# Kernel tuning notes

Measured on AMD Instinct MI355X. Metric: run time of the kernel, lower is better.

## Reference

```python
import jax, jax.numpy as jnp
import numpy as np

EPS = 1e-6
SCAL = 5.0
PARTS = 16
NFEAT = 32
RES = 64


def conv(x, w, b, stride=1):
    y = jax.lax.conv_general_dilated(x, w, (stride, stride), 'SAME',
                                     dimension_numbers=('NCHW', 'OIHW', 'NCHW'))
    return y + b[None, :, None, None]


def spatial_softmax(x):
    b, k, h, w = x.shape
    return jax.nn.softmax(x.reshape(b, k, h * w), axis=-1).reshape(b, k, h, w)


def make_grid(h, w):
    ys = jnp.linspace(-1.0, 1.0, h)
    xs = jnp.linspace(-1.0, 1.0, w)
    gy, gx = jnp.meshgrid(ys, xs, indexing='ij')
    return jnp.stack([gy, gx], axis=-1)  # [h, w, 2]


def e_sigma(x, w1, b1, w2, b2, wp, bp):
    # shared shape/appearance encoder: parts via spatial softmax + residual sum map
    h1 = jax.nn.relu(conv(x, w1, b1, stride=2))   # [B,64,64,64]
    h2 = jax.nn.relu(conv(h1, w2, b2))            # [B,64,64,64]
    parts = spatial_softmax(conv(h2, wp, bp))     # [B,16,64,64]
    return parts, h2


def e_alpha(x, w1, b1, w2, b2):
    h1 = jax.nn.relu(conv(x, w1, b1))
    return conv(h1, w2, b2)                       # [B,32,64,64]


def get_mu_and_prec(parts):
    # soft-argmax mean + 2x2 covariance -> inverse Cholesky factor L_inv
    b, k, h, w = parts.shape
    grid = make_grid(h, w)
    mu = jnp.einsum('bkhw,hwc->bkc', parts, grid)                       # [b,k,2]
    outer = jnp.einsum('hwm,hwn->hwmn', grid, grid)
    cov = jnp.einsum('bkhw,hwmn->bkmn', parts, outer) - jnp.einsum('bkm,bkn->bkmn', mu, mu)
    a = jnp.sqrt(cov[..., 0, 0] + EPS)
    bb = cov[..., 0, 1] / (a + EPS)
    c = jnp.sqrt(jnp.maximum(cov[..., 1, 1] - bb * bb, 0.0) + EPS)
    det = a * c
    z = jnp.zeros_like(a)
    L_inv = SCAL / (det[..., None, None] + EPS) * jnp.stack(
        [jnp.stack([c, z], axis=-1), jnp.stack([-bb, a], axis=-1)], axis=-2)  # [b,k,2,2]
    return mu, L_inv


def feat_mu_to_enc(alpha, mu, L_inv, h, w):
    # render Cauchy-shaped part heatmaps from (mu, L_inv) and paint part features
    grid = make_grid(h, w)
    dist = grid[None, None] - mu[:, :, None, None, :]        # [b,k,h,w,2]
    proj = jnp.einsum('bkhwi,bkij->bkhwj', dist, L_inv)
    heat = 1.0 / (1.0 + jnp.sum(proj * proj, axis=-1))       # [b,k,h,w]
    norm = heat / (jnp.sum(heat, axis=(2, 3), keepdims=True) + EPS)
    fmap = jnp.einsum('bkf,bkhw->bfhw', alpha, norm)         # [b,nf,h,w]
    return jnp.concatenate([heat, fmap], axis=1)             # [b,nk+nf,h,w]


def decoder(enc, w1, b1, w2, b2, w3, b3):
    h1 = jax.nn.relu(conv(enc, w1, b1))                      # [B,64,64,64]
    up = jnp.repeat(jnp.repeat(h1, 2, axis=2), 2, axis=3)    # nearest upsample -> 128
    h2 = jax.nn.relu(conv(up, w2, b2))
    return jax.nn.sigmoid(conv(h2, w3, b3))                  # [B,3,128,128]


def setup_inputs():
    key = jax.random.key(0)
    ks = jax.random.split(key, 16)
    def w(k, shape):
        fan_in = shape[1] * shape[2] * shape[3]
        return (jax.random.normal(k, shape, jnp.float32) / np.sqrt(fan_in)).astype(jnp.float32)
    B = 32
    return {
        'x': jax.random.uniform(ks[0], (B, 3, 128, 128), jnp.float32),
        'x_spatial_transform': jax.random.uniform(ks[1], (B, 3, 128, 128), jnp.float32),
        'x_appearance_transform': jax.random.uniform(ks[2], (B, 3, 128, 128), jnp.float32),
        'coord': jax.random.normal(ks[3], (B, PARTS, 2), jnp.float32) * 0.5,
        'vector': jax.random.normal(ks[4], (B, PARTS, 2), jnp.float32) * 0.1,
        'es_w1': w(ks[5], (RES, 3, 3, 3)), 'es_b1': jnp.zeros((RES,), jnp.float32),
        'es_w2': w(ks[6], (RES, RES, 3, 3)), 'es_b2': jnp.zeros((RES,), jnp.float32),
        'es_wp': w(ks[7], (PARTS, RES, 3, 3)), 'es_bp': jnp.zeros((PARTS,), jnp.float32),
        'ea_w1': w(ks[8], (RES, RES, 3, 3)), 'ea_b1': jnp.zeros((RES,), jnp.float32),
        'ea_w2': w(ks[9], (NFEAT, RES, 3, 3)), 'ea_b2': jnp.zeros((NFEAT,), jnp.float32),
        'd_w1': w(ks[10], (RES, PARTS + NFEAT, 3, 3)), 'd_b1': jnp.zeros((RES,), jnp.float32),
        'd_w2': w(ks[11], (32, RES, 3, 3)), 'd_b2': jnp.zeros((32,), jnp.float32),
        'd_w3': w(ks[12], (3, 32, 3, 3)), 'd_b3': jnp.zeros((3,), jnp.float32),
    }


def reference(x, x_spatial_transform, x_appearance_transform, coord, vector,
              es_w1, es_b1, es_w2, es_b2, es_wp, es_bp,
              ea_w1, ea_b1, ea_w2, ea_b2,
              d_w1, d_b1, d_w2, d_b2, d_w3, d_b3):
    # shape stream (appearance-transformed image -> geometry)
    shape_parts, _ = e_sigma(x_appearance_transform, es_w1, es_b1, es_w2, es_b2, es_wp, es_bp)
    mu, L_inv = get_mu_and_prec(shape_parts)
    # appearance stream (spatially-transformed image -> appearance)
    app_parts, app_sum = e_sigma(x_spatial_transform, es_w1, es_b1, es_w2, es_b2, es_wp, es_bp)
    f_xs = e_alpha(app_sum, ea_w1, ea_b1, ea_w2, ea_b2)
    # local part appearances: gather features under each part map
    alpha = jnp.einsum('bfhw,bkhw->bkf', f_xs, app_parts)
    encoding = feat_mu_to_enc(alpha, mu, L_inv, 64, 64)
    reconstruction = decoder(encoding, d_w1, d_b1, d_w2, d_b2, d_w3, d_b3)
    # composite loss
    mu_a, L_inv_a = get_mu_and_prec(app_parts)
    rec_loss = jnp.mean((x - reconstruction) ** 2)
    equiv_loss = jnp.mean((mu - mu_a) ** 2) + 0.01 * jnp.mean((L_inv - L_inv_a) ** 2)
    transport_loss = jnp.mean((mu_a - (coord + vector)) ** 2)
    loss = rec_loss + equiv_loss + transport_loss
    return reconstruction, loss
```

## Files before the change

### kernel.cpp

```cpp
#include <hip/hip_runtime.h>
#include <hip/hip_bf16.h>

#define EPS 1e-6f
#define SCAL 5.0f

typedef __attribute__((ext_vector_type(8))) short bf8v;
typedef __attribute__((ext_vector_type(4))) float f32x4;

#define OFF_MU     0
#define OFF_LINV   1024
#define OFF_MUA    3072
#define OFF_LINVA  4096
#define OFF_HSUM   6144
#define OFF_ALPHA  6656
#define OFF_REC    23040
#define OFF_R1     32768
#define OFF_R2     (OFF_R1 + 8388608)
#define OFF_R3     (OFF_R2 + 8388608)
#define WS_TOTAL   (OFF_R3 + 16777216)

#define BA_XA   ((size_t)2 * OFF_R3)
#define BA_X2   ((size_t)2 * OFF_R1)
#define OFF_PARTSF OFF_R2
#define OFF_PROBS  (OFF_R2 + 4194304)
#define BA_EA1  ((size_t)2 * OFF_R3)
#define OFF_FXS (OFF_R3 + 4194304)
#define BA_E    ((size_t)2 * OFF_R2)
#define BA_D1   ((size_t)2 * OFF_R1)
#define BA_D2   ((size_t)2 * OFF_R3)

#define WT_ESW1 0
#define WT_ESB1 1728
#define WT_ESB2 1792
#define WT_ESBP 1856
#define WT_EAB1 1872
#define WT_EAB2 1936
#define WT_DB1  1968
#define WT_DB2  2032
#define WT_W3P  2064
#define WT_DB3  2928
#define P_WP2  0
#define P_WPP  36864
#define P_WPA1 46080
#define P_WPA2 82944
#define P_WPD1 101376
#define P_WPD2 138240

__device__ __attribute__((aligned(16))) float g_ws[WS_TOTAL];
__device__ __attribute__((aligned(16))) float g_wt[3072];
__device__ __attribute__((aligned(16))) __hip_bfloat16 g_wp[156672];
__device__ int g_isbf16;

__device__ __forceinline__ float selz(bool c, float v) { return c ? v : 0.f; }
__device__ __forceinline__ float cvtbf(short s) {
    return __uint_as_float(((unsigned int)(unsigned short)s) << 16);
}
__device__ __forceinline__ float ldin(const void* p, size_t i, int bf) {
    return bf ? __bfloat162float(((const __hip_bfloat16*)p)[i])
              : ((const float*)p)[i];
}

__device__ __forceinline__ float block_sum(float v) {
    __shared__ float sb[8];
    for (int off = 32; off; off >>= 1) v += __shfl_down(v, off, 64);
    int lane = threadIdx.x & 63, wid = threadIdx.x >> 6;
    __syncthreads();
    if (lane == 0) sb[wid] = v;
    __syncthreads();
    float r = 0.f;
    for (int i = 0; i < 4; ++i) r += sb[i];
    return r;
}
__device__ __forceinline__ float block_max(float v) {
    __shared__ float sb[8];
    for (int off = 32; off; off >>= 1) v = fmaxf(v, __shfl_down(v, off, 64));
    int lane = threadIdx.x & 63, wid = threadIdx.x >> 6;
    __syncthreads();
    if (lane == 0) sb[wid] = v;
    __syncthreads();
    float r = -1e30f;
    for (int i = 0; i < 4; ++i) r = fmaxf(r, sb[i]);
    return r;
}

__global__ void detect_k(const void* x) {
    const __hip_bfloat16* p = (const __hip_bfloat16*)x;
    int lane = threadIdx.x & 63;
    float v = 0.f;
    for (int i = lane; i < 256; i += 64) {
        float a = fabsf(__bfloat162float(p[i]));
        if (!(a <= 2.0f)) v = 1.f;
    }
    for (int off = 32; off; off >>= 1) v += __shfl_down(v, off, 64);
    if (lane == 0) {
        g_isbf16 = (v == 0.f) ? 1 : 0;
        g_ws[OFF_REC] = 0.f;
    }
}

__global__ void wpack_k(const void* esw1, const void* esb1, const void* esw2, const void* esb2,
                        const void* eswp, const void* esbp, const void* eaw1, const void* eab1,
                        const void* eaw2, const void* eab2, const void* dw1, const void* db1,
                        const void* dw2, const void* db2, const void* dw3, const void* db3) {
    int bf = g_isbf16;
    int gid0 = blockIdx.x * 256 + threadIdx.x, stride = gridDim.x * 256;
    for (int g = gid0; g < 1728; g += stride) g_wt[WT_ESW1 + g] = ldin(esw1, g, bf);
    for (int g = gid0; g < 64; g += stride) g_wt[WT_ESB1 + g] = ldin(esb1, g, bf);
    for (int g = gid0; g < 64; g += stride) g_wt[WT_ESB2 + g] = ldin(esb2, g, bf);
    for (int g = gid0; g < 16; g += stride) g_wt[WT_ESBP + g] = ldin(esbp, g, bf);
    for (int g = gid0; g < 64; g += stride) g_wt[WT_EAB1 + g] = ldin(eab1, g, bf);
    for (int g = gid0; g < 32; g += stride) g_wt[WT_EAB2 + g] = ldin(eab2, g, bf);
    for (int g = gid0; g < 64; g += stride) g_wt[WT_DB1 + g] = ldin(db1, g, bf);
    for (int g = gid0; g < 32; g += stride) g_wt[WT_DB2 + g] = ldin(db2, g, bf);
    for (int g = gid0; g < 3; g += stride) g_wt[WT_DB3 + g] = ldin(db3, g, bf);
    for (int g = gid0; g < 864; g += stride) {
        int t = g / 96, o = (g / 32) % 3, k = g & 31;
        g_wt[WT_W3P + g] = ldin(dw3, (size_t)(o * 32 + k) * 9 + t, bf);
    }
    for (int g = gid0; g < 36864; g += stride) {
        int t = g >> 12, n = (g >> 6) & 63, k = g & 63;
        g_wp[P_WP2 + g] = __float2bfloat16(ldin(esw2, (size_t)(n * 64 + k) * 9 + t, bf));
    }
    for (int g = gid0; g < 9216; g += stride) {
        int t = g >> 10, n = (g >> 6) & 15, k = g & 63;
        g_wp[P_WPP + g] = __float2bfloat16(ldin(eswp, (size_t)(n * 64 + k) * 9 + t, bf));
    }
    for (int g = gid0; g < 36864; g += stride) {
        int t = g >> 12, n = (g >> 6) & 63, k = g & 63;
        g_wp[P_WPA1 + g] = __float2bfloat16(ldin(eaw1, (size_t)(n * 64 + k) * 9 + t, bf));
    }
    for (int g = gid0; g < 18432; g += stride) {
        int t = g >> 11, n = (g >> 6) & 31, k = g & 63;
        g_wp[P_WPA2 + g] = __float2bfloat16(ldin(eaw2, (size_t)(n * 64 + k) * 9 + t, bf));
    }
    for (int g = gid0; g < 36864; g += stride) {
        int t = g >> 12, n = (g >> 6) & 63, k = g & 63;
        float v = (k < 48) ? ldin(dw1, (size_t)(n * 48 + k) * 9 + t, bf) : 0.f;
        g_wp[P_WPD1 + g] = __float2bfloat16(v);
    }
    for (int g = gid0; g < 18432; g += stride) {
        int t = g >> 11, n = (g >> 6) & 31, k = g & 63;
        g_wp[P_WPD2 + g] = __float2bfloat16(ldin(dw2, (size_t)(n * 64 + k) * 9 + t, bf));
    }
}

__global__ void __launch_bounds__(256)
conv_s2n_k(const void* __restrict__ inA, const void* __restrict__ inB) {
    int bf = g_isbf16;
    int tile = blockIdx.x & 15;
    int gb = blockIdx.x >> 4;
    int g = gb & 3, b = gb >> 2;
    const void* in = (b < 32) ? inA : inB;
    int bb = b & 31;
    int pix = tile * 256 + threadIdx.x;
    int y = pix >> 6, x = pix & 63;
    size_t inb = (size_t)bb * 3 * 16384;
    const float* W = g_wt + WT_ESW1 + (size_t)(g * 16) * 27;
    float acc[16];
    #pragma unroll
    for (int o = 0; o < 16; ++o) acc[o] = g_wt[WT_ESB1 + g * 16 + o];
    int iy0 = 2 * y, ix0 = 2 * x;
    bool my2 = (iy0 + 2 < 128), mx2 = (ix0 + 2 < 128);
    int iy2 = my2 ? iy0 + 2 : 127, ix2 = mx2 ? ix0 + 2 : 127;
    for (int ic = 0; ic < 3; ++ic) {
        size_t pb = inb + ic * 16384;
        float t[9];
        t[0] = ldin(in, pb + iy0 * 128 + ix0, bf);
        t[1] = ldin(in, pb + iy0 * 128 + ix0 + 1, bf);
        t[2] = selz(mx2, ldin(in, pb + iy0 * 128 + ix2, bf));
        t[3] = ldin(in, pb + (iy0 + 1) * 128 + ix0, bf);
        t[4] = ldin(in, pb + (iy0 + 1) * 128 + ix0 + 1, bf);
        t[5] = selz(mx2, ldin(in, pb + (iy0 + 1) * 128 + ix2, bf));
        t[6] = selz(my2, ldin(in, pb + iy2 * 128 + ix0, bf));
        t[7] = selz(my2, ldin(in, pb + iy2 * 128 + ix0 + 1, bf));
        t[8] = selz(my2 && mx2, ldin(in, pb + iy2 * 128 + ix2, bf));
        #pragma unroll
        for (int o = 0; o < 16; ++o) {
            const float* wr = W + (o * 3 + ic) * 9;
            float a = acc[o];
            #pragma unroll
            for (int j = 0; j < 9; ++j) a = fmaf(t[j], wr[j], a);
            acc[o] = a;
        }
    }
    __hip_bfloat16* out = (__hip_bfloat16*)g_ws + BA_XA + ((size_t)b * 4096 + pix) * 64 + g * 16;
    #pragma unroll
    for (int o = 0; o < 16; ++o) out[o] = __float2bfloat16(fmaxf(acc[o], 0.f));
}

__device__ __forceinline__ void stage_tile(__hip_bfloat16* sA,
                                           const __hip_bfloat16* __restrict__ inb, int y0) {
    for (int g = threadIdx.x; g < 3072; g += 256) {
        int r = g >> 9;
        int rem = g & 511;
        int px = rem >> 3, j = rem & 7;
        int yy = y0 - 1 + r;
        int P = px + 1;
        bf8v v = (bf8v){0, 0, 0, 0, 0, 0, 0, 0};
        if (yy >= 0 && yy <= 63)
            v = *(const bf8v*)(inb + ((size_t)(yy * 64 + px) * 64 + j * 8));
        *(bf8v*)(sA + ((r * 66 + P) * 64 + ((j ^ (P & 7)) * 8))) = v;
    }
    if (threadIdx.x < 96) {
        int g = threadIdx.x;
        int r = g / 16, rem = g % 16, side = rem >> 3, j = rem & 7;
        int P = side ? 65 : 0;
        *(bf8v*)(sA + ((r * 66 + P) * 64 + ((j ^ (P & 7)) * 8))) = (bf8v){0, 0, 0, 0, 0, 0, 0, 0};
    }
}

template<int TOTN, int NS, int OUTF32, int RELU>
__device__ __forceinline__ void conv_body(const __hip_bfloat16* sA, int bO, int y,
                                          int wid, int l15, int quad,
                                          int wp_off, int bias_off, size_t out_off) {
    f32x4 acc[4][NS];
    #pragma unroll
    for (int ms = 0; ms < 4; ++ms)
        #pragma unroll
        for (int ns = 0; ns < NS; ++ns) acc[ms][ns] = (f32x4){0.f, 0.f, 0.f, 0.f};

    if constexpr (NS == 1) {
        bf8v bw[18];
        #pragma unroll
        for (int it = 0; it < 18; ++it) {
            const int t = it >> 1, c = it & 1;
            bw[it] = *(const bf8v*)(g_wp + wp_off +
                     ((size_t)(t * TOTN + l15) * 64 + c * 32 + quad * 8));
        }
        #pragma unroll
        for (int it = 0; it < 18; ++it) {
            const int t = it >> 1, c = it & 1;
            const int dy = t / 3 - 1, dx = t % 3 - 1;
            const int r = wid + 1 + dy;
            const int j = c * 4 + quad;
            #pragma unroll
            for (int ms = 0; ms < 4; ++ms) {
                int P = ms * 16 + l15 + dx + 1;
                bf8v a = *(const bf8v*)(sA + ((r * 66 + P) * 64 + ((j ^ (P & 7)) * 8)));
                acc[ms][0] = __builtin_amdgcn_mfma_f32_16x16x32_bf16(a, bw[it], acc[ms][0], 0, 0, 0);
            }
        }
    } else {
        bf8v bq[2][NS];
        #pragma unroll
        for (int ns = 0; ns < NS; ++ns)
            bq[0][ns] = *(const bf8v*)(g_wp + wp_off +
                        ((size_t)(ns * 16 + l15) * 64 + quad * 8));
        #pragma unroll
        for (int it = 0; it < 18; ++it) {
            const int t = it >> 1, c = it & 1;
            if (it + 1 < 18) {
                const int t2 = (it + 1) >> 1, c2 = (it + 1) & 1;
                #pragma unroll
                for (int ns = 0; ns < NS; ++ns)
                    bq[(it + 1) & 1][ns] = *(const bf8v*)(g_wp + wp_off +
                        ((size_t)(t2 * TOTN + ns * 16 + l15) * 64 + c2 * 32 + quad * 8));
            }
            const int dy = t / 3 - 1, dx = t % 3 - 1;
            const int r = wid + 1 + dy;
            const int j = c * 4 + quad;
            bf8v a[4];
            #pragma unroll
            for (int ms = 0; ms < 4; ++ms) {
                int P = ms * 16 + l15 + dx + 1;
                a[ms] = *(const bf8v*)(sA + ((r * 66 + P) * 64 + ((j ^ (P & 7)) * 8)));
            }
            #pragma unroll
            for (int ns = 0; ns < NS; ++ns)
                #pragma unroll
                for (int ms = 0; ms < 4; ++ms)
                    acc[ms][ns] = __builtin_amdgcn_mfma_f32_16x16x32_bf16(a[ms], bq[it & 1][ns], acc[ms][ns], 0, 0, 0);
        }
    }

    #pragma unroll
    for (int ns = 0; ns < NS; ++ns) {
        float bias = g_wt[bias_off + ns * 16 + l15];
        #pragma unroll
        for (int ms = 0; ms < 4; ++ms) {
            #pragma unroll
            for (int r = 0; r < 4; ++r) {
                int pix = ms * 16 + quad * 4 + r;
                float v = acc[ms][ns][r] + bias;
                if (RELU) v = fmaxf(v, 0.f);
                size_t o = out_off + ((size_t)(bO * 4096 + y * 64 + pix)) * TOTN + ns * 16 + l15;
                if (OUTF32) g_ws[o] = v;
                else ((__hip_bfloat16*)g_ws)[o] = __float2bfloat16(v);
            }
        }
    }
}

template<int TOTN, int NS, int OUTF32, int RELU>
__global__ void __launch_bounds__(256) __attribute__((amdgpu_waves_per_eu(2, 4)))
conv_mfl_k(size_t in_off, int wp_off, int bias_off, size_t out_off) {
    __shared__ __hip_bfloat16 sA[6 * 66 * 64];
    int wid = threadIdx.x >> 6, lane = threadIdx.x & 63;
    int l15 = lane & 15, quad = lane >> 4;
    int b = blockIdx.x >> 4, y0 = (blockIdx.x & 15) * 4;
    const __hip_bfloat16* inb = (const __hip_bfloat16*)g_ws + in_off + (size_t)b * 4096 * 64;
    stage_tile(sA, inb, y0);
    __syncthreads();
    conv_body<TOTN, NS, OUTF32, RELU>(sA, b, y0 + wid, wid, l15, quad,
                                      wp_off, bias_off, out_off);
}

__global__ void __launch_bounds__(256) __attribute__((amdgpu_waves_per_eu(2, 4)))
conv_pea_k() {
    __shared__ __hip_bfloat16 sA[6 * 66 * 64];
    int wid = threadIdx.x >> 6, lane = threadIdx.x & 63;
    int l15 = lane & 15, quad = lane >> 4;
    int b = blockIdx.x >> 4, y0 = (blockIdx.x & 15) * 4;
    const __hip_bfloat16* inb = (const __hip_bfloat16*)g_ws + BA_X2 + (size_t)b * 4096 * 64;
    stage_tile(sA, inb, y0);
    __syncthreads();
    int y = y0 + wid;
    conv_body<16, 1, 1, 0>(sA, b, y, wid, l15, quad, P_WPP, WT_ESBP, (size_t)OFF_PARTSF);
    if (b >= 32)
        conv_body<64, 4, 0, 1>(sA, b - 32, y, wid, l15, quad, P_WPA1, WT_EAB1, BA_EA1);
}

__global__ void __launch_bounds__(256) __attribute__((amdgpu_waves_per_eu(2, 4)))
conv_upmf2_k(size_t in_off, int wp_off, int bias_off, size_t out_off) {
    __shared__ __hip_bfloat16 sA[4 * 66 * 64];
    int wid = threadIdx.x >> 6, lane = threadIdx.x & 63;
    int l15 = lane & 15, quad = lane >> 4;
    int b = blockIdx.x >> 5, y0 = (blockIdx.x & 31) * 4;
    int ri0 = (y0 >> 1) - 1;
    const __hip_bfloat16* inb = (const __hip_bfloat16*)g_ws + in_off + (size_t)b * 4096 * 64;
    for (int g = threadIdx.x; g < 2048; g += 256) {
        int r = g >> 9;
        int rem = g & 511;
        int px = rem >> 3, j = rem & 7;
        int yi = ri0 + r;
        int P = px + 1;
        bf8v v = (bf8v){0, 0, 0, 0, 0, 0, 0, 0};
        if (yi >= 0 && yi <= 63)
            v = *(const bf8v*)(inb + ((size_t)(yi * 64 + px) * 64 + j * 8));
        *(bf8v*)(sA + ((r * 66 + P) * 64 + ((j ^ (P & 7)) * 8))) = v;
    }
    if (threadIdx.x < 64) {
        int g = threadIdx.x;
        int r = g >> 4, rem = g & 15, side = rem >> 3, j = rem & 7;
        int P = side ? 65 : 0;
        *(bf8v*)(sA + ((r * 66 + P) * 64 + ((j ^ (P & 7)) * 8))) = (bf8v){0, 0, 0, 0, 0, 0, 0, 0};
    }
    __syncthreads();
    int y = y0 + wid;
    f32x4 acc[8][2];
    #pragma unroll
    for (int ms = 0; ms < 8; ++ms)
        #pragma unroll
        for (int ns = 0; ns < 2; ++ns) acc[ms][ns] = (f32x4){0.f, 0.f, 0.f, 0.f};
    bf8v bq[2][2];
    #pragma unroll
    for (int ns = 0; ns < 2; ++ns)
        bq[0][ns] = *(const bf8v*)(g_wp + wp_off + ((size_t)(ns * 16 + l15) * 64 + quad * 8));
    #pragma unroll
    for (int it = 0; it < 18; ++it) {
        const int t = it >> 1, c = it & 1;
        if (it + 1 < 18) {
            const int t2 = (it + 1) >> 1, c2 = (it + 1) & 1;
            #pragma unroll
            for (int ns = 0; ns < 2; ++ns)
                bq[(it + 1) & 1][ns] = *(const bf8v*)(g_wp + wp_off +
                    ((size_t)(t2 * 32 + ns * 16 + l15) * 64 + c2 * 32 + quad * 8));
        }
        const int dy = t / 3 - 1, dx = t % 3 - 1;
        int yy = y + dy;
        if (yy >= 0 && yy <= 127) {
            int r = (yy >> 1) - ri0;
            int j = c * 4 + quad;
            bf8v a[8];
            #pragma unroll
            for (int ms = 0; ms < 8; ++ms) {
                int xx = ms * 16 + l15 + dx;
                int P = (xx < 0) ? 0 : ((xx > 127) ? 65 : ((xx >> 1) + 1));
                a[ms] = *(const bf8v*)(sA + ((r * 66 + P) * 64 + ((j ^ (P & 7)) * 8)));
            }
            #pragma unroll
            for (int ns = 0; ns < 2; ++ns)
                #pragma unroll
                for (int ms = 0; ms < 8; ++ms)
                    acc[ms][ns] = __builtin_amdgcn_mfma_f32_16x16x32_bf16(a[ms], bq[it & 1][ns], acc[ms][ns], 0, 0, 0);
        }
    }
    #pragma unroll
    for (int ns = 0; ns < 2; ++ns) {
        float bias = g_wt[bias_off + ns * 16 + l15];
        #pragma unroll
        for (int ms = 0; ms < 8; ++ms) {
            #pragma unroll
            for (int r = 0; r < 4; ++r) {
                int pix = ms * 16 + quad * 4 + r;
                float v = fmaxf(acc[ms][ns][r] + bias, 0.f);
                size_t o = out_off + ((size_t)(b * 16384 + y * 128 + pix)) * 32 + ns * 16 + l15;
                ((__hip_bfloat16*)g_ws)[o] = __float2bfloat16(v);
            }
        }
    }
}

__global__ void sm_mom3_k() {
    int bk = blockIdx.x;
    int b = bk >> 4, k = bk & 15;
    int app = (b >= 32);
    const float* P = g_ws + OFF_PARTSF + (size_t)b * 4096 * 16 + k;
    float r[16];
    #pragma unroll
    for (int j = 0; j < 16; ++j) r[j] = P[(size_t)(threadIdx.x + j * 256) * 16];
    float m = r[0];
    #pragma unroll
    for (int j = 1; j < 16; ++j) m = fmaxf(m, r[j]);
    m = block_max(m);
    float s = 0.f;
    #pragma unroll
    for (int j = 0; j < 16; ++j) { r[j] = __expf(r[j] - m); s += r[j]; }
    s = block_sum(s);
    float inv = 1.0f / s;
    float sy = 0, sx = 0, syy = 0, sxy = 0, sxx = 0;
    #pragma unroll
    for (int j = 0; j < 16; ++j) {
        float pv = r[j] * inv;
        int i = threadIdx.x + j * 256;
        if (app) g_ws[OFF_PROBS + ((size_t)(b - 32) * 16 + k) * 4096 + i] = pv;
        float gy = -1.0f + (i >> 6) * (2.0f / 63.0f);
        float gx = -1.0f + (i & 63) * (2.0f / 63.0f);
        sy += pv * gy; sx += pv * gx;
        syy += pv * gy * gy; sxy += pv * gy * gx; sxx += pv * gx * gx;
    }
    sy = block_sum(sy); sx = block_sum(sx);
    syy = block_sum(syy); sxy = block_sum(sxy); sxx = block_sum(sxx);
    if (threadIdx.x == 0) {
        float c00 = syy - sy * sy, c01 = sxy - sy * sx, c11 = sxx - sx * sx;
        float a = sqrtf(fmaxf(c00 + EPS, 1e-12f));
        float bb = c01 / (a + EPS);
        float cc = sqrtf(fmaxf(c11 - bb * bb, 0.f) + EPS);
        float det = a * cc;
        float sc = SCAL / (det + EPS);
        int idx = app ? ((b - 32) * 16 + k) : (b * 16 + k);
        int mu_off = app ? OFF_MUA : OFF_MU;
        int linv_off = app ? OFF_LINVA : OFF_LINV;
        g_ws[mu_off + idx * 2 + 0] = sy;
        g_ws[mu_off + idx * 2 + 1] = sx;
        g_ws[linv_off + idx * 4 + 0] = cc * sc;
        g_ws[linv_off + idx * 4 + 1] = 0.f;
        g_ws[linv_off + idx * 4 + 2] = -bb * sc;
        g_ws[linv_off + idx * 4 + 3] = a * sc;
    }
}

__global__ void alpha2_k() {
    int bk = blockIdx.x;
    int b = bk >> 4;
    __shared__ float pl[4096];
    const float* pr = g_ws + OFF_PROBS + (size_t)bk * 4096;
    for (int i = threadIdx.x; i < 4096; i += 256) pl[i] = pr[i];
    __syncthreads();
    float acc[32];
    #pragma unroll
    for (int f = 0; f < 32; ++f) acc[f] = 0.f;
    for (int i = threadIdx.x; i < 4096; i += 256) {
        float pv = pl[i];
        const float* fp = g_ws + OFF_FXS + (size_t)(b * 4096 + i) * 32;
        #pragma unroll
        for (int f = 0; f < 32; ++f) acc[f] = fmaf(pv, fp[f], acc[f]);
    }
    __shared__ float sw[4][32];
    int lane = threadIdx.x & 63, wid = threadIdx.x >> 6;
    #pragma unroll
    for (int f = 0; f < 32; ++f)
        for (int off = 32; off; off >>= 1) acc[f] += __shfl_down(acc[f], off, 64);
    if (lane == 0) {
        #pragma unroll
        for (int f = 0; f < 32; ++f) sw[wid][f] = acc[f];
    }
    __syncthreads();
    if (threadIdx.x < 32)
        g_ws[OFF_ALPHA + bk * 32 + threadIdx.x] =
            sw[0][threadIdx.x] + sw[1][threadIdx.x] + sw[2][threadIdx.x] + sw[3][threadIdx.x];
}

__global__ void heat2_k() {
    int bk = blockIdx.x;
    int b = bk >> 4, k = bk & 15;
    float m0 = g_ws[OFF_MU + bk * 2], m1 = g_ws[OFF_MU + bk * 2 + 1];
    float L00 = g_ws[OFF_LINV + bk * 4 + 0], L10 = g_ws[OFF_LINV + bk * 4 + 2],
          L11 = g_ws[OFF_LINV + bk * 4 + 3];
    __hip_bfloat16* E = (__hip_bfloat16*)g_ws + BA_E;
    float s = 0.f;
    for (int i = threadIdx.x; i < 4096; i += 256) {
        float d0 = -1.0f + (i >> 6) * (2.0f / 63.0f) - m0;
        float d1 = -1.0f + (i & 63) * (2.0f / 63.0f) - m1;
        float p0 = d0 * L00 + d1 * L10;
        float p1 = d1 * L11;
        float h = 1.0f / (1.0f + p0 * p0 + p1 * p1);
        E[(size_t)(b * 4096 + i) * 64 + k] = __float2bfloat16(h);
        s += h;
    }
    s = block_sum(s);
    if (threadIdx.x == 0) g_ws[OFF_HSUM + bk] = s;
}

__global__ void fmap2_k() {
    int tile = blockIdx.x & 15, b = blockIdx.x >> 4;
    __shared__ float coef[16][32];
    for (int i = threadIdx.x; i < 512; i += 256) {
        int k = i >> 5, f = i & 31;
        coef[k][f] = g_ws[OFF_ALPHA + (b * 16 + k) * 32 + f] /
                     (g_ws[OFF_HSUM + b * 16 + k] + EPS);
    }
    __syncthreads();
    int pix = tile * 256 + threadIdx.x;
    __hip_bfloat16* E = (__hip_bfloat16*)g_ws + BA_E + (size_t)(b * 4096 + pix) * 64;
    float h[16];
    #pragma unroll
    for (int k = 0; k < 16; ++k) h[k] = __bfloat162float(E[k]);
    #pragma unroll
    for (int f = 0; f < 32; ++f) {
        float a = 0.f;
        #pragma unroll
        for (int k = 0; k < 16; ++k) a = fmaf(h[k], coef[k][f], a);
        E[16 + f] = __float2bfloat16(a);
    }
    #pragma unroll
    for (int z = 48; z < 64; ++z) E[z] = __float2bfloat16(0.f);
}

__global__ void __launch_bounds__(256)
conv_sign_k(const void* __restrict__ ximg, void* __restrict__ outp) {
    int bf = g_isbf16;
    int tile = blockIdx.x & 63, b = blockIdx.x >> 6;
    int pix = tile * 256 + threadIdx.x;
    int y = pix >> 7, x = pix & 127;
    const short* D2 = (const short*)((const __hip_bfloat16*)g_ws + BA_D2 + (size_t)b * 16384 * 32);
    float acc[3];
    #pragma unroll
    for (int o = 0; o < 3; ++o) acc[o] = g_wt[WT_DB3 + o];
    #pragma unroll
    for (int t = 0; t < 9; ++t) {
        int dy = t / 3 - 1, dx = t % 3 - 1;
        int yy = y + dy, xx = x + dx;
        if (yy < 0 || yy > 127 || xx < 0 || xx > 127) continue;
        const short* sp = D2 + (size_t)(yy * 128 + xx) * 32;
        #pragma unroll
        for (int c = 0; c < 4; ++c) {
            bf8v v = *(const bf8v*)(sp + c * 8);
            #pragma unroll
            for (int j = 0; j < 8; ++j) {
                float av = cvtbf(v[j]);
                int k = c * 8 + j;
                acc[0] = fmaf(av, g_wt[WT_W3P + (t * 3 + 0) * 32 + k], acc[0]);
                acc[1] = fmaf(av, g_wt[WT_W3P + (t * 3 + 1) * 32 + k], acc[1]);
                acc[2] = fmaf(av, g_wt[WT_W3P + (t * 3 + 2) * 32 + k], acc[2]);
            }
        }
    }
    float es = 0.f;
    #pragma unroll
    for (int o = 0; o < 3; ++o) {
        float v = 1.0f / (1.0f + __expf(-acc[o]));
        size_t oidx = ((size_t)b * 3 + o) * 16384 + pix;
        if (bf) ((__hip_bfloat16*)outp)[oidx] = __float2bfloat16(v);
        else    ((float*)outp)[oidx] = v;
        float e = ldin(ximg, oidx, bf) - v;
        es += e * e;
    }
    float s = block_sum(es);
    if (threadIdx.x == 0) atomicAdd(&g_ws[OFF_REC], s);
}

__global__ void loss_k(const void* __restrict__ coord,
                       const void* __restrict__ vec,
                       void* __restrict__ outp) {
    int bf = g_isbf16;
    const float* mu = g_ws + OFF_MU;
    const float* linv = g_ws + OFF_LINV;
    const float* mu_a = g_ws + OFF_MUA;
    const float* linv_a = g_ws + OFF_LINVA;
    float s1 = 0, s2 = 0, s3 = 0;
    for (int i = threadIdx.x; i < 1024; i += 256) {
        float d = mu[i] - mu_a[i];
        s1 += d * d;
        float t = ldin(coord, i, bf) + ldin(vec, i, bf);
        float d3 = mu_a[i] - t;
        s3 += d3 * d3;
    }
    for (int i = threadIdx.x; i < 2048; i += 256) {
        float d = linv[i] - linv_a[i];
        s2 += d * d;
    }
    s1 = block_sum(s1);
    s2 = block_sum(s2);
    s3 = block_sum(s3);
    if (threadIdx.x == 0) {
        float loss = g_ws[OFF_REC] / 1572864.0f + s1 / 1024.0f + 0.01f * (s2 / 2048.0f)
                   + s3 / 1024.0f;
        if (bf) ((__hip_bfloat16*)outp)[1572864] = __float2bfloat16(loss);
        else    ((float*)outp)[1572864] = loss;
    }
}

extern "C" void kernel_launch(void* const* d_in, const int* in_sizes, int n_in,
                              void* d_out, int out_size, void* d_ws, size_t ws_size,
                              hipStream_t stream) {
    const void* x     = d_in[0];
    const void* x_st  = d_in[1];
    const void* x_at  = d_in[2];
    const void* coord = d_in[3];
    const void* vec   = d_in[4];

    dim3 blk(256);

    detect_k<<<1, 64, 0, stream>>>(x);
    wpack_k<<<64, blk, 0, stream>>>(
        d_in[5],  d_in[6],  d_in[7],  d_in[8],
        d_in[9],  d_in[10], d_in[11], d_in[12],
        d_in[13], d_in[14], d_in[15], d_in[16],
        d_in[17], d_in[18], d_in[19], d_in[20]);

    conv_s2n_k<<<64 * 4 * 16, blk, 0, stream>>>(x_at, x_st);
    conv_mfl_k<64, 4, 0, 1><<<1024, blk, 0, stream>>>(BA_XA, P_WP2, WT_ESB2, BA_X2);

    conv_pea_k<<<1024, blk, 0, stream>>>();
    sm_mom3_k<<<1024, blk, 0, stream>>>();

    conv_mfl_k<32, 2, 1, 0><<<512, blk, 0, stream>>>(BA_EA1, P_WPA2, WT_EAB2, (size_t)OFF_FXS);
    alpha2_k<<<512, blk, 0, stream>>>();

    heat2_k<<<512, blk, 0, stream>>>();
    fmap2_k<<<512, blk, 0, stream>>>();

    conv_mfl_k<64, 4, 0, 1><<<512, blk, 0, stream>>>(BA_E, P_WPD1, WT_DB1, BA_D1);
    conv_upmf2_k<<<1024, blk, 0, stream>>>(BA_D1, P_WPD2, WT_DB2, BA_D2);
    conv_sign_k<<<32 * 64, blk, 0, stream>>>(x, d_out);

    loss_k<<<1, blk, 0, stream>>>(coord, vec, d_out);
}
```

Baseline: 452.2 us.

## Halve conv row tiles, split rows across wave pairs, vectorize heatmap writes

The MFMA conv kernels now process 2 output rows per block instead of 4, with each wave covering half a row (32 pixels). This doubles the grid size and shrinks shared memory to raise occupancy. The cost is more halo re-staging, since 4 staged rows feed 2 output rows. The heatmap kernel is restructured so each thread computes all 16 parts for one pixel and writes them as packed 16-byte bf16 vectors, replacing strided 2-byte scatters. Its per-part sums are now accumulated with atomics into a buffer zeroed in the weight-pack kernel. The alpha kernel's block-to-(b,k) mapping is also permuted.

```diff
diff --git a/kernel.cpp b/kernel.cpp
--- a/kernel.cpp
+++ b/kernel.cpp
@@ -55,6 +55,11 @@
 __device__ __forceinline__ float cvtbf(short s) {
     return __uint_as_float(((unsigned int)(unsigned short)s) << 16);
 }
+__device__ __forceinline__ short f2bf(float f) {
+    unsigned u = __float_as_uint(f);
+    u += 0x7fff + ((u >> 16) & 1);
+    return (short)(u >> 16);
+}
 __device__ __forceinline__ float ldin(const void* p, size_t i, int bf) {
     return bf ? __bfloat162float(((const __hip_bfloat16*)p)[i])
               : ((const float*)p)[i];
@@ -104,6 +109,7 @@
                         const void* dw2, const void* db2, const void* dw3, const void* db3) {
     int bf = g_isbf16;
     int gid0 = blockIdx.x * 256 + threadIdx.x, stride = gridDim.x * 256;
+    for (int g = gid0; g < 512; g += stride) g_ws[OFF_HSUM + g] = 0.f;
     for (int g = gid0; g < 1728; g += stride) g_wt[WT_ESW1 + g] = ldin(esw1, g, bf);
     for (int g = gid0; g < 64; g += stride) g_wt[WT_ESB1 + g] = ldin(esb1, g, bf);
     for (int g = gid0; g < 64; g += stride) g_wt[WT_ESB2 + g] = ldin(esb2, g, bf);
@@ -188,9 +194,10 @@
     for (int o = 0; o < 16; ++o) out[o] = __float2bfloat16(fmaxf(acc[o], 0.f));
 }
 
+template<int TR>
 __device__ __forceinline__ void stage_tile(__hip_bfloat16* sA,
                                            const __hip_bfloat16* __restrict__ inb, int y0) {
-    for (int g = threadIdx.x; g < 3072; g += 256) {
+    for (int g = threadIdx.x; g < TR * 512; g += 256) {
         int r = g >> 9;
         int rem = g & 511;
         int px = rem >> 3, j = rem & 7;
@@ -201,24 +208,17 @@
             v = *(const bf8v*)(inb + ((size_t)(yy * 64 + px) * 64 + j * 8));
         *(bf8v*)(sA + ((r * 66 + P) * 64 + ((j ^ (P & 7)) * 8))) = v;
     }
-    if (threadIdx.x < 96) {
+    if (threadIdx.x < TR * 16) {
         int g = threadIdx.x;
-        int r = g / 16, rem = g % 16, side = rem >> 3, j = rem & 7;
+        int r = g >> 4, rem = g & 15, side = rem >> 3, j = rem & 7;
         int P = side ? 65 : 0;
         *(bf8v*)(sA + ((r * 66 + P) * 64 + ((j ^ (P & 7)) * 8))) = (bf8v){0, 0, 0, 0, 0, 0, 0, 0};
     }
 }
 
-template<int TOTN, int NS, int OUTF32, int RELU>
-__device__ __forceinline__ void conv_body(const __hip_bfloat16* sA, int bO, int y,
-                                          int wid, int l15, int quad,
-                                          int wp_off, int bias_off, size_t out_off) {
-    f32x4 acc[4][NS];
-    #pragma unroll
-    for (int ms = 0; ms < 4; ++ms)
-        #pragma unroll
-        for (int ns = 0; ns < NS; ++ns) acc[ms][ns] = (f32x4){0.f, 0.f, 0.f, 0.f};
-
+template<int TOTN, int NS, int MS>
+__device__ __forceinline__ void body18(const __hip_bfloat16* sA, int rowIn, int pxb,
+                                       int l15, int quad, int wp_off, f32x4 (&acc)[MS][NS]) {
     if constexpr (NS == 1) {
         bf8v bw[18];
         #pragma unroll
@@ -231,11 +231,11 @@
         for (int it = 0; it < 18; ++it) {
             const int t = it >> 1, c = it & 1;
             const int dy = t / 3 - 1, dx = t % 3 - 1;
-            const int r = wid + 1 + dy;
+            const int r = rowIn + 1 + dy;
             const int j = c * 4 + quad;
             #pragma unroll
-            for (int ms = 0; ms < 4; ++ms) {
-                int P = ms * 16 + l15 + dx + 1;
+            for (int ms = 0; ms < MS; ++ms) {
+                int P = pxb + ms * 16 + l15 + dx + 1;
                 bf8v a = *(const bf8v*)(sA + ((r * 66 + P) * 64 + ((j ^ (P & 7)) * 8)));
                 acc[ms][0] = __builtin_amdgcn_mfma_f32_16x16x32_bf16(a, bw[it], acc[ms][0], 0, 0, 0);
             }
@@ -257,30 +257,34 @@
                         ((size_t)(t2 * TOTN + ns * 16 + l15) * 64 + c2 * 32 + quad * 8));
             }
             const int dy = t / 3 - 1, dx = t % 3 - 1;
-            const int r = wid + 1 + dy;
+            const int r = rowIn + 1 + dy;
             const int j = c * 4 + quad;
-            bf8v a[4];
-            #pragma unroll
-            for (int ms = 0; ms < 4; ++ms) {
-                int P = ms * 16 + l15 + dx + 1;
+            bf8v a[MS];
+            #pragma unroll
+            for (int ms = 0; ms < MS; ++ms) {
+                int P = pxb + ms * 16 + l15 + dx + 1;
                 a[ms] = *(const bf8v*)(sA + ((r * 66 + P) * 64 + ((j ^ (P & 7)) * 8)));
             }
             #pragma unroll
             for (int ns = 0; ns < NS; ++ns)
                 #pragma unroll
-                for (int ms = 0; ms < 4; ++ms)
+                for (int ms = 0; ms < MS; ++ms)
                     acc[ms][ns] = __builtin_amdgcn_mfma_f32_16x16x32_bf16(a[ms], bq[it & 1][ns], acc[ms][ns], 0, 0, 0);
         }
     }
-
+}
+
+template<int TOTN, int NS, int MS, int OUTF32, int RELU>
+__device__ __forceinline__ void epi_std(f32x4 (&acc)[MS][NS], int bO, int y, int pxb,
+                                        int l15, int quad, int bias_off, size_t out_off) {
     #pragma unroll
     for (int ns = 0; ns < NS; ++ns) {
         float bias = g_wt[bias_off + ns * 16 + l15];
         #pragma unroll
-        for (int ms = 0; ms < 4; ++ms) {
+        for (int ms = 0; ms < MS; ++ms) {
             #pragma unroll
             for (int r = 0; r < 4; ++r) {
-                int pix = ms * 16 + quad * 4 + r;
+                int pix = pxb + ms * 16 + quad * 4 + r;
                 float v = acc[ms][ns][r] + bias;
                 if (RELU) v = fmaxf(v, 0.f);
                 size_t o = out_off + ((size_t)(bO * 4096 + y * 64 + pix)) * TOTN + ns * 16 + l15;
@@ -292,32 +296,52 @@
 }
 
 template<int TOTN, int NS, int OUTF32, int RELU>
-__global__ void __launch_bounds__(256) __attribute__((amdgpu_waves_per_eu(2, 4)))
-conv_mfl_k(size_t in_off, int wp_off, int bias_off, size_t out_off) {
-    __shared__ __hip_bfloat16 sA[6 * 66 * 64];
+__global__ void __launch_bounds__(256, 4)
+conv_mfl3_k(size_t in_off, int wp_off, int bias_off, size_t out_off) {
+    __shared__ __hip_bfloat16 sA[4 * 66 * 64];
     int wid = threadIdx.x >> 6, lane = threadIdx.x & 63;
     int l15 = lane & 15, quad = lane >> 4;
-    int b = blockIdx.x >> 4, y0 = (blockIdx.x & 15) * 4;
+    int b = blockIdx.x >> 5, y0 = (blockIdx.x & 31) * 2;
+    int rowIn = wid >> 1, pxb = (wid & 1) * 32;
+    int y = y0 + rowIn;
     const __hip_bfloat16* inb = (const __hip_bfloat16*)g_ws + in_off + (size_t)b * 4096 * 64;
-    stage_tile(sA, inb, y0);
-    __syncthreads();
-    conv_body<TOTN, NS, OUTF32, RELU>(sA, b, y0 + wid, wid, l15, quad,
-                                      wp_off, bias_off, out_off);
-}
-
-__global__ void __launch_bounds__(256) __attribute__((amdgpu_waves_per_eu(2, 4)))
-conv_pea_k() {
-    __shared__ __hip_bfloat16 sA[6 * 66 * 64];
+    stage_tile<4>(sA, inb, y0);
+    __syncthreads();
+    f32x4 acc[2][NS];
+    #pragma unroll
+    for (int ms = 0; ms < 2; ++ms)
+        #pragma unroll
+        for (int ns = 0; ns < NS; ++ns) acc[ms][ns] = (f32x4){0.f, 0.f, 0.f, 0.f};
+    body18<TOTN, NS, 2>(sA, rowIn, pxb, l15, quad, wp_off, acc);
+    epi_std<TOTN, NS, 2, OUTF32, RELU>(acc, b, y, pxb, l15, quad, bias_off, out_off);
+}
+
+__global__ void __launch_bounds__(256, 4)
+conv_pea3_k() {
+    __shared__ __hip_bfloat16 sA[4 * 66 * 64];
     int wid = threadIdx.x >> 6, lane = threadIdx.x & 63;
     int l15 = lane & 15, quad = lane >> 4;
-    int b = blockIdx.x >> 4, y0 = (blockIdx.x & 15) * 4;
+    int b = blockIdx.x >> 5, y0 = (blockIdx.x & 31) * 2;
+    int rowIn = wid >> 1, pxb = (wid & 1) * 32;
+    int y = y0 + rowIn;
+    int app = (b >= 32);
     const __hip_bfloat16* inb = (const __hip_bfloat16*)g_ws + BA_X2 + (size_t)b * 4096 * 64;
-    stage_tile(sA, inb, y0);
-    __syncthreads();
-    int y = y0 + wid;
-    conv_body<16, 1, 1, 0>(sA, b, y, wid, l15, quad, P_WPP, WT_ESBP, (size_t)OFF_PARTSF);
-    if (b >= 32)
-        conv_body<64, 4, 0, 1>(sA, b - 32, y, wid, l15, quad, P_WPA1, WT_EAB1, BA_EA1);
+    stage_tile<4>(sA, inb, y0);
+    __syncthreads();
+    f32x4 accP[2][1];
+    #pragma unroll
+    for (int ms = 0; ms < 2; ++ms) accP[ms][0] = (f32x4){0.f, 0.f, 0.f, 0.f};
+    body18<16, 1, 2>(sA, rowIn, pxb, l15, quad, P_WPP, accP);
+    epi_std<16, 1, 2, 1, 0>(accP, b, y, pxb, l15, quad, WT_ESBP, (size_t)OFF_PARTSF);
+    if (app) {
+        f32x4 accE[2][4];
+        #pragma unroll
+        for (int ms = 0; ms < 2; ++ms)
+            #pragma unroll
+            for (int ns = 0; ns < 4; ++ns) accE[ms][ns] = (f32x4){0.f, 0.f, 0.f, 0.f};
+        body18<64, 4, 2>(sA, rowIn, pxb, l15, quad, P_WPA1, accE);
+        epi_std<64, 4, 2, 0, 1>(accE, b - 32, y, pxb, l15, quad, WT_EAB1, BA_EA1);
+    }
 }
 
 __global__ void __launch_bounds__(256) __attribute__((amdgpu_waves_per_eu(2, 4)))
@@ -451,8 +475,8 @@
 }
 
 __global__ void alpha2_k() {
-    int bk = blockIdx.x;
-    int b = bk >> 4;
+    int b = blockIdx.x & 31, k = blockIdx.x >> 5;
+    int bk = b * 16 + k;
     __shared__ float pl[4096];
     const float* pr = g_ws + OFF_PROBS + (size_t)bk * 4096;
     for (int i = threadIdx.x; i < 4096; i += 256) pl[i] = pr[i];
@@ -482,24 +506,41 @@
 }
 
 __global__ void heat2_k() {
-    int bk = blockIdx.x;
-    int b = bk >> 4, k = bk & 15;
-    float m0 = g_ws[OFF_MU + bk * 2], m1 = g_ws[OFF_MU + bk * 2 + 1];
-    float L00 = g_ws[OFF_LINV + bk * 4 + 0], L10 = g_ws[OFF_LINV + bk * 4 + 2],
-          L11 = g_ws[OFF_LINV + bk * 4 + 3];
-    __hip_bfloat16* E = (__hip_bfloat16*)g_ws + BA_E;
-    float s = 0.f;
-    for (int i = threadIdx.x; i < 4096; i += 256) {
-        float d0 = -1.0f + (i >> 6) * (2.0f / 63.0f) - m0;
-        float d1 = -1.0f + (i & 63) * (2.0f / 63.0f) - m1;
+    int tile = blockIdx.x & 15, b = blockIdx.x >> 4;
+    __shared__ float hs[16];
+    if (threadIdx.x < 16) hs[threadIdx.x] = 0.f;
+    __syncthreads();
+    int pix = tile * 256 + threadIdx.x;
+    float gy = -1.0f + (pix >> 6) * (2.0f / 63.0f);
+    float gx = -1.0f + (pix & 63) * (2.0f / 63.0f);
+    bf8v e0, e1;
+    float hv[16];
+    #pragma unroll
+    for (int k = 0; k < 16; ++k) {
+        int bk = b * 16 + k;
+        float m0 = g_ws[OFF_MU + bk * 2], m1 = g_ws[OFF_MU + bk * 2 + 1];
+        float L00 = g_ws[OFF_LINV + bk * 4 + 0], L10 = g_ws[OFF_LINV + bk * 4 + 2],
+              L11 = g_ws[OFF_LINV + bk * 4 + 3];
+        float d0 = gy - m0, d1 = gx - m1;
         float p0 = d0 * L00 + d1 * L10;
         float p1 = d1 * L11;
         float h = 1.0f / (1.0f + p0 * p0 + p1 * p1);
-        E[(size_t)(b * 4096 + i) * 64 + k] = __float2bfloat16(h);
-        s += h;
-    }
-    s = block_sum(s);
-    if (threadIdx.x == 0) g_ws[OFF_HSUM + bk] = s;
+        hv[k] = h;
+        short sbits = f2bf(h);
+        if (k < 8) e0[k] = sbits; else e1[k - 8] = sbits;
+    }
+    __hip_bfloat16* E = (__hip_bfloat16*)g_ws + BA_E + (size_t)(b * 4096 + pix) * 64;
+    *(bf8v*)E = e0;
+    *(bf8v*)(E + 8) = e1;
+    #pragma unroll
+    for (int k = 0; k < 16; ++k) {
+        float v = hv[k];
+        for (int off = 32; off; off >>= 1) v += __shfl_down(v, off, 64);
+        if ((threadIdx.x & 63) == 0) atomicAdd(&hs[k], v);
+    }
+    __syncthreads();
+    if (threadIdx.x < 16)
+        atomicAdd(&g_ws[OFF_HSUM + b * 16 + threadIdx.x], hs[threadIdx.x]);
 }
 
 __global__ void fmap2_k() {
@@ -620,18 +661,18 @@
         d_in[17], d_in[18], d_in[19], d_in[20]);
 
     conv_s2n_k<<<64 * 4 * 16, blk, 0, stream>>>(x_at, x_st);
-    conv_mfl_k<64, 4, 0, 1><<<1024, blk, 0, stream>>>(BA_XA, P_WP2, WT_ESB2, BA_X2);
-
-    conv_pea_k<<<1024, blk, 0, stream>>>();
+    conv_mfl3_k<64, 4, 0, 1><<<2048, blk, 0, stream>>>(BA_XA, P_WP2, WT_ESB2, BA_X2);
+
+    conv_pea3_k<<<2048, blk, 0, stream>>>();
     sm_mom3_k<<<1024, blk, 0, stream>>>();
 
-    conv_mfl_k<32, 2, 1, 0><<<512, blk, 0, stream>>>(BA_EA1, P_WPA2, WT_EAB2, (size_t)OFF_FXS);
+    conv_mfl3_k<32, 2, 1, 0><<<1024, blk, 0, stream>>>(BA_EA1, P_WPA2, WT_EAB2, (size_t)OFF_FXS);
     alpha2_k<<<512, blk, 0, stream>>>();
 
     heat2_k<<<512, blk, 0, stream>>>();
     fmap2_k<<<512, blk, 0, stream>>>();
 
-    conv_mfl_k<64, 4, 0, 1><<<512, blk, 0, stream>>>(BA_E, P_WPD1, WT_DB1, BA_D1);
+    conv_mfl3_k<64, 4, 0, 1><<<1024, blk, 0, stream>>>(BA_E, P_WPD1, WT_DB1, BA_D1);
     conv_upmf2_k<<<1024, blk, 0, stream>>>(BA_D1, P_WPD2, WT_DB2, BA_D2);
     conv_sign_k<<<32 * 64, blk, 0, stream>>>(x, d_out);
 
```

Result: slower. 514.2 us (+13.7%).
